# Optimization experiments

Hardware: AMD Instinct MI355X
Metric: run time of the kernel (lower is better)

The kernel has to match this reference:

```python
import jax, jax.numpy as jnp
import numpy as np
from jax.scipy.special import ndtr, logsumexp

K = 2  # top-k experts (init kwarg k=2)


def setup_inputs() -> dict:
    key = jax.random.key(0)
    k1, k2, k3, k4 = jax.random.split(key, 4)
    B, D, E = 131072, 1024, 64
    x_flat = jax.random.normal(k1, (B, D), jnp.float32)
    # Original inits w_gate/w_noise to zeros; use small random weights so
    # top-k routing is non-degenerate for correctness testing.
    w_gate = jax.random.normal(k2, (D, E), jnp.float32) * 0.02
    w_noise = jax.random.normal(k3, (D, E), jnp.float32) * 0.02
    eps = jax.random.normal(k4, (B, E), jnp.float32)  # reified torch.randn_like
    return {"x_flat": x_flat, "w_gate": w_gate, "w_noise": w_noise, "eps": eps}


def _cv_squared(v):
    # torch .var() is unbiased (ddof=1)
    return jnp.var(v, ddof=1) / (jnp.mean(v) ** 2 + 1e-10)


def reference(x_flat, w_gate, w_noise, eps):
    B = x_flat.shape[0]
    clean_logits = x_flat @ w_gate                                  # [B, E]
    noise_stddev = jax.nn.softplus(x_flat @ w_noise) + 0.01         # [B, E]
    logits = clean_logits + eps * noise_stddev                      # noisy logits (training)

    top_vals, top_idx = jax.lax.top_k(logits, K + 1)                # [B, K+1], sorted desc
    top_k_gates = jax.nn.softmax(top_vals[:, :K], axis=-1)          # [B, K]
    gates = jnp.zeros_like(logits).at[jnp.arange(B)[:, None], top_idx[:, :K]].set(top_k_gates)

    # _prob_in_top_k load estimate (noisy gating, k < num_experts, training)
    thr_if_in = top_vals[:, K:K + 1]                                # (k+1)-th largest
    thr_if_out = top_vals[:, K - 1:K]                               # k-th largest
    is_in = logits > thr_if_in
    prob_if_in = ndtr((clean_logits - thr_if_in) / noise_stddev)
    prob_if_out = ndtr((clean_logits - thr_if_out) / noise_stddev)
    load = jnp.where(is_in, prob_if_in, prob_if_out).sum(0)         # [E]

    importance = gates.sum(0)                                       # [E]
    z_loss = logsumexp(logits, axis=-1).mean()                      # log(sum(exp)).mean()
    load_balancing = _cv_squared(importance) + _cv_squared(load) + z_loss
    return gates, load, logits, load_balancing, importance
```

## Files before the change

### kernel.cpp

```cpp
#include <hip/hip_runtime.h>
#include <math.h>

#define B_ROWS 131072
#define D_DIM  1024
#define E_EXP  64
#define MARGIN 4e-3f

typedef _Float16 f16;
typedef _Float16 f16x8 __attribute__((ext_vector_type(8)));
typedef float    f32x4 __attribute__((ext_vector_type(4)));

#define AS1C(p) ((const __attribute__((address_space(1))) void*)(p))
#define AS3(p)  ((__attribute__((address_space(3))) void*)(p))


__device__ __forceinline__ float softplus_f(float t) {
  return (t > 20.0f) ? t : log1pf(expf(t));
}
__device__ __forceinline__ float ndtr_f(float z) {
  return 0.5f * erfcf(-z * 0.70710678118654752f);
}
__device__ __forceinline__ void argmax64(float& v, int& vi) {
  #pragma unroll
  for (int off = 32; off > 0; off >>= 1) {
    float ov = __shfl_xor(v, off, 64);
    int   oi = __shfl_xor(vi, off, 64);
    if (ov > v || (ov == v && oi < vi)) { v = ov; vi = oi; }
  }
}
__device__ __forceinline__ float sum64(float v) {
  #pragma unroll
  for (int off = 32; off > 0; off >>= 1) v += __shfl_xor(v, off, 64);
  return v;
}

__device__ __forceinline__ void row_epilogue_exact(
    int row, int lane, float clean, float sd, float l,
    float* __restrict__ gates_buf, float* __restrict__ logits_buf,
    float& load_acc, float& imp_acc, float& z_acc)
{
  float v1 = l; int i1 = lane; argmax64(v1, i1);
  float v2 = (lane == i1) ? -INFINITY : l; int i2 = lane; argmax64(v2, i2);
  float v3 = (lane == i1 || lane == i2) ? -INFINITY : l; int i3 = lane; argmax64(v3, i3);
  (void)i3;
  const float e21 = expf(v2 - v1);
  const float g1  = 1.0f / (1.0f + e21);
  const float g2  = e21 * g1;
  const float gv  = (lane == i1) ? g1 : ((lane == i2) ? g2 : 0.0f);
  gates_buf [(size_t)row * E_EXP + lane] = gv;
  logits_buf[(size_t)row * E_EXP + lane] = l;
  const float ssum = sum64(expf(l - v1));
  z_acc += v1 + logf(ssum);
  const float thr = (l > v3) ? v3 : v2;
  load_acc += ndtr_f((clean - thr) / sd);
  imp_acc  += gv;
}


__global__ __launch_bounds__(256) void prep_wt(
    const float* __restrict__ wg, const float* __restrict__ wn, f16* __restrict__ wt,
    float* load_o, float* imp_o, float* zsum, int* flagcnt) {
  if (blockIdx.x == 0) {
    const int t = threadIdx.x;
    if (t < 64) { load_o[t] = 0.0f; imp_o[t] = 0.0f; }
    if (t == 64) zsum[0] = 0.0f;
    if (t == 65) flagcnt[0] = 0;
  }
  __shared__ float tile[64][65];
  const int m  = blockIdx.x >> 4;
  const int kt = blockIdx.x & 15;
  const int k0 = kt * 64;
  const float* src = m ? wn : wg;
  const int c = threadIdx.x & 63;
  const int r0 = threadIdx.x >> 6;
  #pragma unroll
  for (int r = r0; r < 64; r += 4)
    tile[r][c] = src[(size_t)(k0 + r) * 64 + c];
  __syncthreads();
  const int j = threadIdx.x & 63;
  #pragma unroll
  for (int col = r0; col < 64; col += 4)
    wt[(size_t)(m * 64 + col) * 1024 + k0 + j] = (f16)tile[j][col];
}

__global__ __launch_bounds__(256, 2) void gemm_fused(
    const float* __restrict__ x, const f16* __restrict__ wt,
    const float* __restrict__ eps,
    float* __restrict__ gates_buf, float* __restrict__ logits_buf,
    float* __restrict__ load_o, float* __restrict__ imp_o, float* __restrict__ zsum,
    int* __restrict__ flagcnt, int* __restrict__ flaglist)
{
  __shared__ __align__(16) char xlds[2][16384];
  __shared__ __align__(16) char blds[2][16384];
  __shared__ float red[520];

  const int tid  = threadIdx.x;
  const int lane = tid & 63;
  const int wid  = tid >> 6;
  const int l15  = lane & 15;
  const int l4   = lane >> 4;
  const size_t brow0   = (size_t)blockIdx.x * 64;
  const size_t rowbase = brow0 + wid * 16;

  const int scol0 = wid * 8 + (lane >> 3);
  const int skel  = ((lane & 7) * 8) ^ ((lane >> 3) << 3);
  const f16* wsrc0 = wt + (size_t)(scol0 +  0) * 1024 + skel;
  const f16* wsrc1 = wt + (size_t)(scol0 + 32) * 1024 + skel;
  const f16* wsrc2 = wt + (size_t)(scol0 + 64) * 1024 + skel;
  const f16* wsrc3 = wt + (size_t)(scol0 + 96) * 1024 + skel;

  const int xr0 = lane >> 3;
  const int xc  = lane & 7;
  const float* xrowp0 = x + (brow0 + wid * 16 + xr0) * D_DIM;
  const float* xrowp1 = xrowp0 + 8 * D_DIM;
  const int plo = (xc ^ xr0) * 4;
  const int phi = plo + 32;
  const float* xsrc00 = xrowp0 + plo;
  const float* xsrc01 = xrowp0 + phi;
  const float* xsrc10 = xrowp1 + phi;
  const float* xsrc11 = xrowp1 + plo;

#define STAGE(buf, kc) do {                                                                              \
    __builtin_amdgcn_global_load_lds(AS1C(wsrc0  + (kc) * 64), AS3(&blds[buf][0*4096 + wid*1024]), 16, 0, 0); \
    __builtin_amdgcn_global_load_lds(AS1C(wsrc1  + (kc) * 64), AS3(&blds[buf][1*4096 + wid*1024]), 16, 0, 0); \
    __builtin_amdgcn_global_load_lds(AS1C(wsrc2  + (kc) * 64), AS3(&blds[buf][2*4096 + wid*1024]), 16, 0, 0); \
    __builtin_amdgcn_global_load_lds(AS1C(wsrc3  + (kc) * 64), AS3(&blds[buf][3*4096 + wid*1024]), 16, 0, 0); \
    __builtin_amdgcn_global_load_lds(AS1C(xsrc00 + (kc) * 64), AS3(&xlds[buf][0*8192 + (wid*16 + 0)*128]), 16, 0, 0); \
    __builtin_amdgcn_global_load_lds(AS1C(xsrc01 + (kc) * 64), AS3(&xlds[buf][1*8192 + (wid*16 + 0)*128]), 16, 0, 0); \
    __builtin_amdgcn_global_load_lds(AS1C(xsrc10 + (kc) * 64), AS3(&xlds[buf][0*8192 + (wid*16 + 8)*128]), 16, 0, 0); \
    __builtin_amdgcn_global_load_lds(AS1C(xsrc11 + (kc) * 64), AS3(&xlds[buf][1*8192 + (wid*16 + 8)*128]), 16, 0, 0); \
  } while (0)

  f32x4 acc[8];
  #pragma unroll
  for (int et = 0; et < 8; ++et) acc[et] = (f32x4)0.0f;

  STAGE(0, 0);
  __syncthreads();

  #pragma unroll 1
  for (int kc = 0; kc < 16; ++kc) {
    const int buf = kc & 1;

    if (kc < 15) STAGE(buf ^ 1, kc + 1);

    f16x8 af[2];
    #pragma unroll
    for (int kl = 0; kl < 2; ++kl) {
      #pragma unroll
      for (int s = 0; s < 2; ++s) {
        const int pl  = kl * 8 + l4 * 2 + s;
        const int pp  = pl ^ l15;
        const int off = ((pp & 8) << 10) | ((wid * 16 + l15) << 7) | ((pp & 7) << 4);
        const float4 v = *(const float4*)(&xlds[buf][off]);
        af[kl][s*4 + 0] = (f16)v.x;
        af[kl][s*4 + 1] = (f16)v.y;
        af[kl][s*4 + 2] = (f16)v.z;
        af[kl][s*4 + 3] = (f16)v.w;
      }
    }

    #pragma unroll
    for (int kl = 0; kl < 2; ++kl) {
      #pragma unroll
      for (int et = 0; et < 8; ++et) {
        const int bcol = et * 16 + l15;
        const int boff = (bcol * 128 + kl * 64 + l4 * 16) ^ ((l15 & 7) << 4);
        const f16x8 b = *(const f16x8*)(&blds[buf][boff]);
        acc[et] = __builtin_amdgcn_mfma_f32_16x16x32_f16(af[kl], b, acc[et], 0, 0, 0);
      }
    }

    __syncthreads();
  }
#undef STAGE

  float load_acc[4] = {0.f, 0.f, 0.f, 0.f};
  float imp_acc[4]  = {0.f, 0.f, 0.f, 0.f};
  float z_acc = 0.f;

  #pragma unroll
  for (int rg = 0; rg < 4; ++rg) {
    const size_t row = rowbase + l4 * 4 + rg;
    float cl[4], sd[4], lg[4];
    #pragma unroll
    for (int j = 0; j < 4; ++j) {
      cl[j] = acc[j][rg];
      sd[j] = softplus_f(acc[4 + j][rg]) + 0.01f;
      const float ev = eps[row * E_EXP + j * 16 + l15];
      lg[j] = fmaf(ev, sd[j], cl[j]);
    }
    float v = lg[0]; int c = l15;
    #pragma unroll
    for (int j = 1; j < 4; ++j) {
      const int cj = j * 16 + l15;
      if (lg[j] > v || (lg[j] == v && cj < c)) { v = lg[j]; c = cj; }
    }
    #pragma unroll
    for (int off = 1; off < 16; off <<= 1) {
      const float ov = __shfl_xor(v, off, 64);
      const int   oc = __shfl_xor(c, off, 64);
      if (ov > v || (ov == v && oc < c)) { v = ov; c = oc; }
    }
    const float v1 = v; const int i1 = c;
    v = -INFINITY; c = 1 << 30;
    #pragma unroll
    for (int j = 0; j < 4; ++j) {
      const int cj = j * 16 + l15;
      if (cj != i1 && (lg[j] > v || (lg[j] == v && cj < c))) { v = lg[j]; c = cj; }
    }
    #pragma unroll
    for (int off = 1; off < 16; off <<= 1) {
      const float ov = __shfl_xor(v, off, 64);
      const int   oc = __shfl_xor(c, off, 64);
      if (ov > v || (ov == v && oc < c)) { v = ov; c = oc; }
    }
    const float v2 = v; const int i2 = c;
    float v3 = -INFINITY;
    #pragma unroll
    for (int j = 0; j < 4; ++j) {
      const int cj = j * 16 + l15;
      if (cj != i1 && cj != i2) v3 = fmaxf(v3, lg[j]);
    }
    #pragma unroll
    for (int off = 1; off < 16; off <<= 1) v3 = fmaxf(v3, __shfl_xor(v3, off, 64));

    if (v2 - v3 >= MARGIN) {
      const float e21 = expf(v2 - v1);
      const float g1  = 1.0f / (1.0f + e21);
      const float g2  = e21 * g1;
      float s = 0.f;
      #pragma unroll
      for (int j = 0; j < 4; ++j) s += expf(lg[j] - v1);
      #pragma unroll
      for (int off = 1; off < 16; off <<= 1) s += __shfl_xor(s, off, 64);
      if (l15 == 0) z_acc += v1 + logf(s);
      #pragma unroll
      for (int j = 0; j < 4; ++j) {
        const int cj = j * 16 + l15;
        const float gv = (cj == i1) ? g1 : ((cj == i2) ? g2 : 0.0f);
        gates_buf [row * E_EXP + cj] = gv;
        logits_buf[row * E_EXP + cj] = lg[j];
        imp_acc[j] += gv;
        const float thr = (lg[j] > v3) ? v3 : v2;
        load_acc[j] += ndtr_f((cl[j] - thr) / sd[j]);
      }
    } else {
      if (l15 == 0) { const int idx = atomicAdd(flagcnt, 1); flaglist[idx] = (int)row; }
    }
  }

  #pragma unroll
  for (int j = 0; j < 4; ++j) {
    float L = load_acc[j]; L += __shfl_xor(L, 16, 64); L += __shfl_xor(L, 32, 64);
    float I = imp_acc[j];  I += __shfl_xor(I, 16, 64); I += __shfl_xor(I, 32, 64);
    if (l4 == 0) {
      red[wid * 64 + j * 16 + l15]       = L;
      red[256 + wid * 64 + j * 16 + l15] = I;
    }
  }
  {
    const float zw = sum64(z_acc);
    if (lane == 0) red[512 + wid] = zw;
  }
  __syncthreads();
  if (wid == 0) {
    const float L = red[lane] + red[64 + lane] + red[128 + lane] + red[192 + lane];
    const float I = red[256 + lane] + red[320 + lane] + red[384 + lane] + red[448 + lane];
    atomicAdd(&load_o[lane], L);
    atomicAdd(&imp_o[lane],  I);
    if (lane == 0) atomicAdd(zsum, red[512] + red[513] + red[514] + red[515]);
  }
}

__global__ __launch_bounds__(256) void fixup_k(
    const float* __restrict__ x, const float* __restrict__ wg, const float* __restrict__ wn,
    const float* __restrict__ eps,
    float* __restrict__ gates_buf, float* __restrict__ logits_buf,
    float* __restrict__ load_o, float* __restrict__ imp_o, float* __restrict__ zsum,
    const int* __restrict__ flagcnt, const int* __restrict__ flaglist)
{
  const int lane = threadIdx.x & 63;
  const int wid  = threadIdx.x >> 6;
  __shared__ float redg[4][4][64], redn[4][4][64];

  const int nf = *flagcnt;

  for (int it = blockIdx.x * 4; it < nf; it += gridDim.x * 4) {
    const int nr = (nf - it < 4) ? (nf - it) : 4;
    int rows[4];
    #pragma unroll
    for (int rr = 0; rr < 4; ++rr) rows[rr] = flaglist[it + ((rr < nr) ? rr : 0)];

    float dg[4] = {0.f,0.f,0.f,0.f}, dn[4] = {0.f,0.f,0.f,0.f};
    const int dbase = wid * 256;
    for (int d = 0; d < 256; d += 4) {
      const int db = (dbase + d) * E_EXP + lane;
      const float wgv0 = wg[db], wgv1 = wg[db + 64], wgv2 = wg[db + 128], wgv3 = wg[db + 192];
      const float wnv0 = wn[db], wnv1 = wn[db + 64], wnv2 = wn[db + 128], wnv3 = wn[db + 192];
      #pragma unroll
      for (int rr = 0; rr < 4; ++rr) {
        const float4 xv = *(const float4*)(x + (size_t)rows[rr] * D_DIM + dbase + d);
        dg[rr] = fmaf(xv.x, wgv0, dg[rr]);  dn[rr] = fmaf(xv.x, wnv0, dn[rr]);
        dg[rr] = fmaf(xv.y, wgv1, dg[rr]);  dn[rr] = fmaf(xv.y, wnv1, dn[rr]);
        dg[rr] = fmaf(xv.z, wgv2, dg[rr]);  dn[rr] = fmaf(xv.z, wnv2, dn[rr]);
        dg[rr] = fmaf(xv.w, wgv3, dg[rr]);  dn[rr] = fmaf(xv.w, wnv3, dn[rr]);
      }
    }
    #pragma unroll
    for (int rr = 0; rr < 4; ++rr) { redg[wid][rr][lane] = dg[rr]; redn[wid][rr][lane] = dn[rr]; }
    __syncthreads();
    if (wid < nr) {
      const int row = rows[wid];
      const float clean = redg[0][wid][lane] + redg[1][wid][lane] + redg[2][wid][lane] + redg[3][wid][lane];
      const float sdraw = redn[0][wid][lane] + redn[1][wid][lane] + redn[2][wid][lane] + redn[3][wid][lane];
      const float sd = softplus_f(sdraw) + 0.01f;
      const float ev = eps[(size_t)row * E_EXP + lane];
      const float l  = fmaf(ev, sd, clean);
      float la = 0.f, ia = 0.f, za = 0.f;
      row_epilogue_exact(row, lane, clean, sd, l, gates_buf, logits_buf, la, ia, za);
      atomicAdd(&load_o[lane], la);
      atomicAdd(&imp_o[lane],  ia);
      if (lane == 0) atomicAdd(zsum, za);
    }
    __syncthreads();
  }
}

__global__ void finalize_k(const float* __restrict__ load_o,
                           const float* __restrict__ imp_o,
                           const float* __restrict__ zsum,
                           float* __restrict__ out_lb) {
  const int e = threadIdx.x & 63;
  const double a = (double)load_o[e];
  const double b = (double)imp_o[e];
  double sl = a, sl2 = a * a, si = b, si2 = b * b;
  #pragma unroll
  for (int off = 32; off > 0; off >>= 1) {
    sl  += __shfl_xor(sl,  off, 64);
    sl2 += __shfl_xor(sl2, off, 64);
    si  += __shfl_xor(si,  off, 64);
    si2 += __shfl_xor(si2, off, 64);
  }
  if (e == 0) {
    const double n  = (double)E_EXP;
    const double ml = sl / n, mi = si / n;
    const double varl = (sl2 - n * ml * ml) / (n - 1.0);
    const double vari = (si2 - n * mi * mi) / (n - 1.0);
    const double cvl = varl / (ml * ml + 1e-10);
    const double cvi = vari / (mi * mi + 1e-10);
    const double z  = (double)zsum[0] / (double)B_ROWS;
    out_lb[0] = (float)(cvi + cvl + z);
  }
}


extern "C" void kernel_launch(void* const* d_in, const int* in_sizes, int n_in,
                              void* d_out, int out_size, void* d_ws, size_t ws_size,
                              hipStream_t stream) {
  const float* x   = (const float*)d_in[0];
  const float* wg  = (const float*)d_in[1];
  const float* wn  = (const float*)d_in[2];
  const float* eps = (const float*)d_in[3];

  float* out    = (float*)d_out;
  float* gates  = out;
  float* load_o = out + (size_t)B_ROWS * E_EXP;
  float* logits = load_o + E_EXP;
  float* lb     = logits + (size_t)B_ROWS * E_EXP;
  float* imp    = lb + 1;

  float* zsum     = (float*)d_ws;
  int*   flagcnt  = (int*)d_ws + 2;
  int*   flaglist = (int*)((char*)d_ws + 256);
  f16*   wt       = (f16*)((char*)d_ws + 256 + 4 * (size_t)B_ROWS);

  prep_wt<<<32, 256, 0, stream>>>(wg, wn, wt, load_o, imp, zsum, flagcnt);
  gemm_fused<<<B_ROWS / 64, 256, 0, stream>>>(
      x, wt, eps, gates, logits, load_o, imp, zsum, flagcnt, flaglist);
  fixup_k<<<512, 256, 0, stream>>>(x, wg, wn, eps, gates, logits, load_o, imp, zsum, flagcnt, flaglist);
  finalize_k<<<1, 64, 0, stream>>>(load_o, imp, zsum, lb);
}
```

Before: 278.0 us.

## Triple-buffer x tiles with vmcnt-based waits and swizzle block order

Switches the GEMM mainloop from double-buffered x/w staging with full __syncthreads to a triple-buffered x ring (prefetch two k-chunks ahead) and a double-buffered weight ring, using s_waitcnt vmcnt(4) plus a raw barrier so the newest loads stay in flight across iterations. All LDS is merged into one 80KB array, and the reduction scratch now aliases it after a barrier. Block indices are remapped with a stride-8 swizzle that changes which rows neighbouring workgroups process. LDS per block grows from about 66KB to 80KB, which may limit the two-blocks-per-CU occupancy requested in launch bounds.

```diff
diff --git a/kernel.cpp b/kernel.cpp
--- a/kernel.cpp
+++ b/kernel.cpp
@@ -90,16 +90,17 @@
     float* __restrict__ load_o, float* __restrict__ imp_o, float* __restrict__ zsum,
     int* __restrict__ flagcnt, int* __restrict__ flaglist)
 {
-  __shared__ __align__(16) char xlds[2][16384];
-  __shared__ __align__(16) char blds[2][16384];
-  __shared__ float red[520];
+  __shared__ __align__(16) char lds[81920];
 
   const int tid  = threadIdx.x;
   const int lane = tid & 63;
   const int wid  = tid >> 6;
   const int l15  = lane & 15;
   const int l4   = lane >> 4;
-  const size_t brow0   = (size_t)blockIdx.x * 64;
+
+  const int nwg = (int)gridDim.x;
+  const int swz = (blockIdx.x & 7) * (nwg >> 3) + (blockIdx.x >> 3);
+  const size_t brow0   = (size_t)swz * 64;
   const size_t rowbase = brow0 + wid * 16;
 
   const int scol0 = wid * 8 + (lane >> 3);
@@ -120,60 +121,81 @@
   const float* xsrc10 = xrowp1 + phi;
   const float* xsrc11 = xrowp1 + plo;
 
-#define STAGE(buf, kc) do {                                                                              \
-    __builtin_amdgcn_global_load_lds(AS1C(wsrc0  + (kc) * 64), AS3(&blds[buf][0*4096 + wid*1024]), 16, 0, 0); \
-    __builtin_amdgcn_global_load_lds(AS1C(wsrc1  + (kc) * 64), AS3(&blds[buf][1*4096 + wid*1024]), 16, 0, 0); \
-    __builtin_amdgcn_global_load_lds(AS1C(wsrc2  + (kc) * 64), AS3(&blds[buf][2*4096 + wid*1024]), 16, 0, 0); \
-    __builtin_amdgcn_global_load_lds(AS1C(wsrc3  + (kc) * 64), AS3(&blds[buf][3*4096 + wid*1024]), 16, 0, 0); \
-    __builtin_amdgcn_global_load_lds(AS1C(xsrc00 + (kc) * 64), AS3(&xlds[buf][0*8192 + (wid*16 + 0)*128]), 16, 0, 0); \
-    __builtin_amdgcn_global_load_lds(AS1C(xsrc01 + (kc) * 64), AS3(&xlds[buf][1*8192 + (wid*16 + 0)*128]), 16, 0, 0); \
-    __builtin_amdgcn_global_load_lds(AS1C(xsrc10 + (kc) * 64), AS3(&xlds[buf][0*8192 + (wid*16 + 8)*128]), 16, 0, 0); \
-    __builtin_amdgcn_global_load_lds(AS1C(xsrc11 + (kc) * 64), AS3(&xlds[buf][1*8192 + (wid*16 + 8)*128]), 16, 0, 0); \
+#define ISSUE_B(bOff, kc) do {                                                                                 \
+    __builtin_amdgcn_global_load_lds(AS1C(wsrc0 + (kc) * 64), AS3(lds + 49152 + (bOff) + 0*4096 + wid*1024), 16, 0, 0); \
+    __builtin_amdgcn_global_load_lds(AS1C(wsrc1 + (kc) * 64), AS3(lds + 49152 + (bOff) + 1*4096 + wid*1024), 16, 0, 0); \
+    __builtin_amdgcn_global_load_lds(AS1C(wsrc2 + (kc) * 64), AS3(lds + 49152 + (bOff) + 2*4096 + wid*1024), 16, 0, 0); \
+    __builtin_amdgcn_global_load_lds(AS1C(wsrc3 + (kc) * 64), AS3(lds + 49152 + (bOff) + 3*4096 + wid*1024), 16, 0, 0); \
   } while (0)
 
+#define ISSUE_X(xOff, kc) do {                                                                                 \
+    __builtin_amdgcn_global_load_lds(AS1C(xsrc00 + (kc) * 64), AS3(lds + (xOff) + 0*8192 + (wid*16 + 0)*128), 16, 0, 0); \
+    __builtin_amdgcn_global_load_lds(AS1C(xsrc01 + (kc) * 64), AS3(lds + (xOff) + 1*8192 + (wid*16 + 0)*128), 16, 0, 0); \
+    __builtin_amdgcn_global_load_lds(AS1C(xsrc10 + (kc) * 64), AS3(lds + (xOff) + 0*8192 + (wid*16 + 8)*128), 16, 0, 0); \
+    __builtin_amdgcn_global_load_lds(AS1C(xsrc11 + (kc) * 64), AS3(lds + (xOff) + 1*8192 + (wid*16 + 8)*128), 16, 0, 0); \
+  } while (0)
+
   f32x4 acc[8];
   #pragma unroll
   for (int et = 0; et < 8; ++et) acc[et] = (f32x4)0.0f;
 
-  STAGE(0, 0);
-  __syncthreads();
+#define COMPUTE(xRdOff, bRdOff) do {                                             \
+    f16x8 af[2];                                                                 \
+    _Pragma("unroll")                                                            \
+    for (int kl = 0; kl < 2; ++kl) {                                             \
+      _Pragma("unroll")                                                          \
+      for (int s = 0; s < 2; ++s) {                                              \
+        const int pl  = kl * 8 + l4 * 2 + s;                                     \
+        const int pp  = pl ^ l15;                                                \
+        const int off = (xRdOff) + ((pp & 8) << 10) + ((wid*16 + l15) << 7) + ((pp & 7) << 4); \
+        const float4 v = *(const float4*)(lds + off);                            \
+        af[kl][s*4 + 0] = (f16)v.x;                                              \
+        af[kl][s*4 + 1] = (f16)v.y;                                              \
+        af[kl][s*4 + 2] = (f16)v.z;                                              \
+        af[kl][s*4 + 3] = (f16)v.w;                                              \
+      }                                                                          \
+    }                                                                            \
+    _Pragma("unroll")                                                            \
+    for (int kl = 0; kl < 2; ++kl) {                                             \
+      _Pragma("unroll")                                                          \
+      for (int et = 0; et < 8; ++et) {                                           \
+        const int bcol = et * 16 + l15;                                          \
+        const int boff = (bRdOff) + ((bcol * 128 + kl * 64 + l4 * 16) ^ ((l15 & 7) << 4)); \
+        const f16x8 b = *(const f16x8*)(lds + boff);                             \
+        acc[et] = __builtin_amdgcn_mfma_f32_16x16x32_f16(af[kl], b, acc[et], 0, 0, 0); \
+      }                                                                          \
+    }                                                                            \
+  } while (0)
+
+  ISSUE_B(0, 0);
+  ISSUE_X(0, 0);
+  ISSUE_X(16384, 1);
+  asm volatile("s_waitcnt vmcnt(4)" ::: "memory");
+  __builtin_amdgcn_s_barrier();
+
+  int xRd = 0, xWr = 32768, bRd = 0, bWr = 16384;
 
   #pragma unroll 1
-  for (int kc = 0; kc < 16; ++kc) {
-    const int buf = kc & 1;
-
-    if (kc < 15) STAGE(buf ^ 1, kc + 1);
-
-    f16x8 af[2];
-    #pragma unroll
-    for (int kl = 0; kl < 2; ++kl) {
-      #pragma unroll
-      for (int s = 0; s < 2; ++s) {
-        const int pl  = kl * 8 + l4 * 2 + s;
-        const int pp  = pl ^ l15;
-        const int off = ((pp & 8) << 10) | ((wid * 16 + l15) << 7) | ((pp & 7) << 4);
-        const float4 v = *(const float4*)(&xlds[buf][off]);
-        af[kl][s*4 + 0] = (f16)v.x;
-        af[kl][s*4 + 1] = (f16)v.y;
-        af[kl][s*4 + 2] = (f16)v.z;
-        af[kl][s*4 + 3] = (f16)v.w;
-      }
-    }
-
-    #pragma unroll
-    for (int kl = 0; kl < 2; ++kl) {
-      #pragma unroll
-      for (int et = 0; et < 8; ++et) {
-        const int bcol = et * 16 + l15;
-        const int boff = (bcol * 128 + kl * 64 + l4 * 16) ^ ((l15 & 7) << 4);
-        const f16x8 b = *(const f16x8*)(&blds[buf][boff]);
-        acc[et] = __builtin_amdgcn_mfma_f32_16x16x32_f16(af[kl], b, acc[et], 0, 0, 0);
-      }
-    }
-
-    __syncthreads();
-  }
-#undef STAGE
+  for (int kc = 0; kc < 14; ++kc) {
+    ISSUE_B(bWr, kc + 1);
+    ISSUE_X(xWr, kc + 2);
+    COMPUTE(xRd, 49152 + bRd);
+    asm volatile("s_waitcnt vmcnt(4)" ::: "memory");
+    __builtin_amdgcn_s_barrier();
+    xRd += 16384; if (xRd == 49152) xRd = 0;
+    xWr += 16384; if (xWr == 49152) xWr = 0;
+    bRd ^= 16384; bWr ^= 16384;
+  }
+  ISSUE_B(bWr, 15);
+  COMPUTE(xRd, 49152 + bRd);
+  asm volatile("s_waitcnt vmcnt(0)" ::: "memory");
+  __builtin_amdgcn_s_barrier();
+  xRd += 16384; if (xRd == 49152) xRd = 0;
+  bRd ^= 16384;
+  COMPUTE(xRd, 49152 + bRd);
+#undef ISSUE_B
+#undef ISSUE_X
+#undef COMPUTE
 
   float load_acc[4] = {0.f, 0.f, 0.f, 0.f};
   float imp_acc[4]  = {0.f, 0.f, 0.f, 0.f};
@@ -250,6 +272,8 @@
     }
   }
 
+  __syncthreads();
+  float* red = (float*)lds;
   #pragma unroll
   for (int j = 0; j < 4; ++j) {
     float L = load_acc[j]; L += __shfl_xor(L, 16, 64); L += __shfl_xor(L, 32, 64);
```

Result: no change. 278.8 us (+0.3%).
